# Optimization experiments

Hardware: AMD Instinct MI355X
Metric: run time of the kernel (lower is better)

## Reference

```python
import jax, jax.numpy as jnp
import numpy as np

N = 100000      # nodes
E = 1600000     # edges (avg degree 16)
D_IN, D_H, D_OUT = 128, 128, 64


def setup_inputs() -> dict:
    key = jax.random.key(0)
    k1, k2, k3, k4 = jax.random.split(key, 4)
    x = jax.random.normal(k1, (N, D_IN), dtype=jnp.float32)
    edge_index = jax.random.randint(k2, (2, E), 0, N, dtype=jnp.int32)
    W1 = jax.random.normal(k3, (D_IN, D_H), dtype=jnp.float32) * (1.0 / np.sqrt(D_IN))
    b1 = jnp.zeros((D_H,), dtype=jnp.float32)
    W2 = jax.random.normal(k4, (D_H, D_OUT), dtype=jnp.float32) * (1.0 / np.sqrt(D_H))
    b2 = jnp.zeros((D_OUT,), dtype=jnp.float32)
    return {"x": x, "edge_index": edge_index, "W1": W1, "b1": b1, "W2": W2, "b2": b2}


def _gcn_conv(x, src, dst, W, b):
    """PyG GCNConv: out = D^{-1/2} (A + I) D^{-1/2} (x W) + b."""
    n = x.shape[0]
    h = x @ W  # [N, D_out] — transform first, then aggregate (PyG order)
    loops = jnp.arange(n, dtype=src.dtype)
    src_f = jnp.concatenate([src, loops])
    dst_f = jnp.concatenate([dst, loops])
    deg = jax.ops.segment_sum(jnp.ones_like(dst_f, dtype=h.dtype), dst_f, num_segments=n)
    dinv = jax.lax.rsqrt(deg)  # deg >= 1 due to self-loops
    norm = dinv[src_f] * dinv[dst_f]            # [E+N]
    msg = h[src_f] * norm[:, None]              # [E+N, D_out] gather
    out = jax.ops.segment_sum(msg, dst_f, num_segments=n)  # scatter-add
    return out + b


def reference(x, edge_index, W1, b1, W2, b2):
    src, dst = edge_index[0], edge_index[1]
    h = jax.nn.relu(_gcn_conv(x, src, dst, W1, b1))
    o = _gcn_conv(h, src, dst, W2, b2)
    return jax.nn.log_softmax(o, axis=1)
```

## Files before the change

### kernel.cpp

```cpp
#include <hip/hip_runtime.h>
#include <hip/hip_bf16.h>

typedef __hip_bfloat16 bf16;
typedef short short8 __attribute__((ext_vector_type(8)));
typedef float f32x4 __attribute__((ext_vector_type(4)));

#define NPB 256
#define MAXBUK 1024

__device__ __forceinline__ float bf2f_raw(unsigned short u) {
    unsigned x = ((unsigned)u) << 16; float f; __builtin_memcpy(&f, &x, 4); return f;
}
__device__ __forceinline__ unsigned short f2bf_raw(float f) {
    unsigned u; __builtin_memcpy(&u, &f, 4);
    u += 0x7FFFu + ((u >> 16) & 1u);
    return (unsigned short)(u >> 16);
}
__device__ __forceinline__ float lo_f(unsigned u) {
    unsigned x = u << 16; float f; __builtin_memcpy(&f, &x, 4); return f;
}
__device__ __forceinline__ float hi_f(unsigned u) {
    unsigned x = u & 0xffff0000u; float f; __builtin_memcpy(&f, &x, 4); return f;
}


__global__ __launch_bounds__(1024) void sniff_kernel(const unsigned short* __restrict__ w,
                                                     int nshorts, int* __restrict__ flag) {
    __shared__ int red[1024];
    const int t = threadIdx.x;
    int c = 0;
    for (int i = t; i < nshorts; i += 1024) {
        unsigned e = (w[i] >> 7) & 0xFFu;
        if (e >= 140u || (e >= 1u && e <= 40u)) c++;
    }
    red[t] = c;
    __syncthreads();
    for (int o = 512; o > 0; o >>= 1) {
        if (t < o) red[t] += red[t + o];
        __syncthreads();
    }
    if (t == 0) *flag = (red[0] > nshorts / 8) ? 1 : 0;
}


__global__ __launch_bounds__(256) void prep_kernel(const void* __restrict__ W1p,
                                                   const void* __restrict__ W2p,
                                                   const void* __restrict__ b1p,
                                                   const void* __restrict__ b2p,
                                                   unsigned short* __restrict__ WB1,
                                                   unsigned short* __restrict__ WB2,
                                                   float* __restrict__ b1f,
                                                   float* __restrict__ b2f,
                                                   const int* __restrict__ flag) {
    const int isf32 = *flag;
    const int t = blockIdx.x * 256 + threadIdx.x;
    const int T1 = 16384, T2 = 8192;
    if (t < T1) {
        int j = t & 7, l = (t >> 3) & 63, f = t >> 9;
        int n = f >> 2, kk = f & 3;
        int k = kk * 32 + (l >> 4) * 8 + j;
        int col = n * 16 + (l & 15);
        WB1[t] = isf32 ? f2bf_raw(((const float*)W1p)[k * 128 + col])
                       : ((const unsigned short*)W1p)[k * 128 + col];
    } else if (t < T1 + T2) {
        int o = t - T1;
        int j = o & 7, l = (o >> 3) & 63, f = o >> 9;
        int n = f >> 2, kk = f & 3;
        int k = kk * 32 + (l >> 4) * 8 + j;
        int col = n * 16 + (l & 15);
        WB2[o] = isf32 ? f2bf_raw(((const float*)W2p)[k * 64 + col])
                       : ((const unsigned short*)W2p)[k * 64 + col];
    } else if (t < T1 + T2 + 128) {
        int o = t - T1 - T2;
        b1f[o] = isf32 ? ((const float*)b1p)[o] : bf2f_raw(((const unsigned short*)b1p)[o]);
    } else if (t < T1 + T2 + 192) {
        int o = t - T1 - T2 - 128;
        b2f[o] = isf32 ? ((const float*)b2p)[o] : bf2f_raw(((const unsigned short*)b2p)[o]);
    }
}


__global__ __launch_bounds__(256) void ms_count_kernel(const int* __restrict__ dst,
                                                       int* __restrict__ bktcnt,
                                                       int E, int nbuk) {
    __shared__ int cnt[MAXBUK];
    const int t = threadIdx.x;
    const int e0 = blockIdx.x * 4096;
    const int e1 = min(E, e0 + 4096);
    for (int b = t; b < nbuk; b += 256) cnt[b] = 0;
    __syncthreads();
    for (int e = e0 + t; e < e1; e += 256) atomicAdd(&cnt[dst[e] >> 8], 1);
    __syncthreads();
    for (int b = t; b < nbuk; b += 256) {
        int c = cnt[b];
        if (c) atomicAdd(&bktcnt[b], c);
    }
}

__global__ __launch_bounds__(1024) void bscan_kernel(const int* __restrict__ bktcnt,
                                                     int* __restrict__ bofs,
                                                     int* __restrict__ bcur,
                                                     int* __restrict__ rofs,
                                                     int nbuk, int n, int total) {
    __shared__ int ps[1024];
    const int t = threadIdx.x;
    int v = (t < nbuk) ? bktcnt[t] : 0;
    ps[t] = v;
    __syncthreads();
    for (int o = 1; o < 1024; o <<= 1) {
        int u = (t >= o) ? ps[t - o] : 0;
        __syncthreads();
        ps[t] += u;
        __syncthreads();
    }
    if (t < nbuk) {
        int ex = ps[t] - v;
        bofs[t] = ex;
        bcur[t] = ex;
    }
    if (t == 0) {
        bofs[nbuk] = total;
        rofs[n] = total;
    }
}

__global__ __launch_bounds__(256) void ms_scatter_kernel(const int* __restrict__ src,
                                                         const int* __restrict__ dst,
                                                         int* __restrict__ bcur,
                                                         unsigned* __restrict__ packed,
                                                         int E, int nbuk) {
    __shared__ int cnt[MAXBUK];
    __shared__ int gbase[MAXBUK];
    const int t = threadIdx.x;
    const int e0 = blockIdx.x * 4096;
    const int e1 = min(E, e0 + 4096);
    for (int b = t; b < nbuk; b += 256) cnt[b] = 0;
    __syncthreads();
    for (int e = e0 + t; e < e1; e += 256) atomicAdd(&cnt[dst[e] >> 8], 1);
    __syncthreads();
    for (int b = t; b < nbuk; b += 256) {
        int c = cnt[b];
        gbase[b] = c ? atomicAdd(&bcur[b], c) : 0;
        cnt[b] = 0;
    }
    __syncthreads();
    for (int e = e0 + t; e < e1; e += 256) {
        int d = dst[e];
        int b = d >> 8;
        int r = atomicAdd(&cnt[b], 1);
        packed[gbase[b] + r] = ((unsigned)(d & 255) << 24) | (unsigned)src[e];
    }
}

__global__ __launch_bounds__(256) void csr_fine2_kernel(const unsigned* __restrict__ packed,
                                                        const int* __restrict__ bofs,
                                                        int* __restrict__ rofs,
                                                        float* __restrict__ dinv,
                                                        int* __restrict__ csrc, int n) {
    __shared__ int cnt2[NPB];
    __shared__ int cur[NPB];
    const int t = threadIdx.x;
    const int b = blockIdx.x;
    const int node0 = b << 8;
    const int nn = min(NPB, n - node0);
    cnt2[t] = 0;
    __syncthreads();
    const int beg = bofs[b], end = bofs[b + 1];
    for (int i = beg + t; i < end; i += 256) atomicAdd(&cnt2[packed[i] >> 24], 1);
    __syncthreads();
    int c = cnt2[t];
    cur[t] = c;
    __syncthreads();
    for (int o = 1; o < 256; o <<= 1) {
        int u = (t >= o) ? cur[t - o] : 0;
        __syncthreads();
        cur[t] += u;
        __syncthreads();
    }
    const int base = beg + cur[t] - c;
    if (t < nn) {
        rofs[node0 + t] = base;
        dinv[node0 + t] = rsqrtf((float)(c + 1));
    }
    __syncthreads();
    cur[t] = base;
    __syncthreads();
    for (int i = beg + t; i < end; i += 256) {
        unsigned u = packed[i];
        int pos = atomicAdd(&cur[u >> 24], 1);
        csrc[pos] = (int)(u & 0xFFFFFFu);
    }
}


__global__ __launch_bounds__(256) void gemm1_mfma(const void* __restrict__ Xp,
                                                  const unsigned short* __restrict__ WB1,
                                                  unsigned short* __restrict__ H, int nrows,
                                                  const int* __restrict__ flag) {
    __shared__ __align__(16) unsigned short Xs[128 * 136];
    __shared__ __align__(16) unsigned short Cs[128 * 68];
    const int t = threadIdx.x;
    const int r0 = blockIdx.x * 128;
    const int isf32 = *flag;

    if (isf32) {
        const float4* Xg = (const float4*)Xp;
        #pragma unroll
        for (int i = 0; i < 16; ++i) {
            int idx = t + 256 * i;
            int row = idx >> 5, c4 = idx & 31;
            float4 v = {0.f, 0.f, 0.f, 0.f};
            if (r0 + row < nrows) v = Xg[(size_t)(r0 + row) * 32 + c4];
            unsigned lo = (unsigned)f2bf_raw(v.x) | ((unsigned)f2bf_raw(v.y) << 16);
            unsigned hi = (unsigned)f2bf_raw(v.z) | ((unsigned)f2bf_raw(v.w) << 16);
            *reinterpret_cast<uint2*>(&Xs[row * 136 + c4 * 4]) = make_uint2(lo, hi);
        }
    } else {
        const uint4* Xg = (const uint4*)Xp;
        #pragma unroll
        for (int i = 0; i < 8; ++i) {
            int idx = t + 256 * i;
            int row = idx >> 4, c8 = idx & 15;
            uint4 v = {0u, 0u, 0u, 0u};
            if (r0 + row < nrows) v = Xg[(size_t)(r0 + row) * 16 + c8];
            *reinterpret_cast<uint4*>(&Xs[row * 136 + c8 * 8]) = v;
        }
    }
    __syncthreads();

    const int lane = t & 63, w = t >> 6;
    const int m0 = w * 32;
    short8 a[2][4];
    #pragma unroll
    for (int rt = 0; rt < 2; ++rt)
        #pragma unroll
        for (int kk = 0; kk < 4; ++kk)
            a[rt][kk] = *reinterpret_cast<const short8*>(
                &Xs[(m0 + rt * 16 + (lane & 15)) * 136 + kk * 32 + (lane >> 4) * 8]);

    for (int p = 0; p < 2; ++p) {
        short8 b[4][4];
        #pragma unroll
        for (int n = 0; n < 4; ++n)
            #pragma unroll
            for (int kk = 0; kk < 4; ++kk)
                b[n][kk] = *reinterpret_cast<const short8*>(
                    WB1 + (size_t)(((p * 4 + n) * 4 + kk) * 64 + lane) * 8);
        f32x4 acc[2][4];
        #pragma unroll
        for (int rt = 0; rt < 2; ++rt)
            #pragma unroll
            for (int n = 0; n < 4; ++n) {
                acc[rt][n] = (f32x4){0.f, 0.f, 0.f, 0.f};
                #pragma unroll
                for (int kk = 0; kk < 4; ++kk)
                    acc[rt][n] = __builtin_amdgcn_mfma_f32_16x16x32_bf16(
                        a[rt][kk], b[n][kk], acc[rt][n], 0, 0, 0);
            }
        if (p) __syncthreads();
        #pragma unroll
        for (int rt = 0; rt < 2; ++rt)
            #pragma unroll
            for (int n = 0; n < 4; ++n)
                #pragma unroll
                for (int r = 0; r < 4; ++r) {
                    int row = m0 + rt * 16 + (lane >> 4) * 4 + r;
                    Cs[row * 68 + n * 16 + (lane & 15)] = f2bf_raw(acc[rt][n][r]);
                }
        __syncthreads();
        #pragma unroll
        for (int i = 0; i < 8; ++i) {
            int idx = t + 256 * i;
            int row = idx >> 4, c4 = idx & 15;
            if (r0 + row < nrows) {
                uint2 v = *reinterpret_cast<const uint2*>(&Cs[row * 68 + c4 * 4]);
                *reinterpret_cast<uint2*>(H + (size_t)(r0 + row) * 128 + p * 64 + c4 * 4) = v;
            }
        }
        if (!p) __syncthreads();
    }
}


template <bool RELU_BIAS>
__global__ __launch_bounds__(256) void agg128_v2(const unsigned* __restrict__ H32,
                                                 const int* __restrict__ rofs,
                                                 const int* __restrict__ csrc,
                                                 const float* __restrict__ dinv,
                                                 const float* __restrict__ biasf,
                                                 unsigned* __restrict__ G32, int n) {
    const int lane = threadIdx.x & 63;
    const int node = blockIdx.x * 4 + (threadIdx.x >> 6);
    if (node >= n) return;
    const float di = dinv[node];
    unsigned u = H32[(size_t)node * 64 + lane];
    const float dii = di * di;
    float a0 = dii * lo_f(u), a1 = dii * hi_f(u);
    int j = rofs[node];
    const int end = rofs[node + 1];
    for (; j + 3 < end; j += 4) {
        int s0 = csrc[j], s1 = csrc[j + 1], s2 = csrc[j + 2], s3 = csrc[j + 3];
        float w0 = di * dinv[s0], w1 = di * dinv[s1];
        float w2 = di * dinv[s2], w3 = di * dinv[s3];
        unsigned v0 = H32[(size_t)s0 * 64 + lane];
        unsigned v1 = H32[(size_t)s1 * 64 + lane];
        unsigned v2 = H32[(size_t)s2 * 64 + lane];
        unsigned v3 = H32[(size_t)s3 * 64 + lane];
        a0 = fmaf(w0, lo_f(v0), a0); a1 = fmaf(w0, hi_f(v0), a1);
        a0 = fmaf(w1, lo_f(v1), a0); a1 = fmaf(w1, hi_f(v1), a1);
        a0 = fmaf(w2, lo_f(v2), a0); a1 = fmaf(w2, hi_f(v2), a1);
        a0 = fmaf(w3, lo_f(v3), a0); a1 = fmaf(w3, hi_f(v3), a1);
    }
    for (; j < end; ++j) {
        int s = csrc[j];
        float w = di * dinv[s];
        unsigned v = H32[(size_t)s * 64 + lane];
        a0 = fmaf(w, lo_f(v), a0);
        a1 = fmaf(w, hi_f(v), a1);
    }
    if (RELU_BIAS) {
        a0 = fmaxf(a0 + biasf[2 * lane], 0.f);
        a1 = fmaxf(a1 + biasf[2 * lane + 1], 0.f);
    }
    G32[(size_t)node * 64 + lane] = (unsigned)f2bf_raw(a0) | ((unsigned)f2bf_raw(a1) << 16);
}


__global__ __launch_bounds__(256) void gemm2_mfma(const unsigned short* __restrict__ X,
                                                  const unsigned short* __restrict__ WB2,
                                                  const float* __restrict__ b2f,
                                                  void* __restrict__ OUTv, int nrows,
                                                  const int* __restrict__ flag) {
    __shared__ __align__(16) unsigned short Xs[128 * 136];
    const int t = threadIdx.x;
    const int r0 = blockIdx.x * 128;
    const int outf32 = *flag;

    const uint4* Xg = (const uint4*)X;
    #pragma unroll
    for (int i = 0; i < 8; ++i) {
        int idx = t + 256 * i;
        int row = idx >> 4, c8 = idx & 15;
        uint4 v = {0u, 0u, 0u, 0u};
        if (r0 + row < nrows) v = Xg[(size_t)(r0 + row) * 16 + c8];
        *reinterpret_cast<uint4*>(&Xs[row * 136 + c8 * 8]) = v;
    }
    __syncthreads();

    const int lane = t & 63, w = t >> 6;
    const int m0 = w * 32;
    short8 a[2][4];
    #pragma unroll
    for (int rt = 0; rt < 2; ++rt)
        #pragma unroll
        for (int kk = 0; kk < 4; ++kk)
            a[rt][kk] = *reinterpret_cast<const short8*>(
                &Xs[(m0 + rt * 16 + (lane & 15)) * 136 + kk * 32 + (lane >> 4) * 8]);

    short8 b[4][4];
    #pragma unroll
    for (int n = 0; n < 4; ++n)
        #pragma unroll
        for (int kk = 0; kk < 4; ++kk)
            b[n][kk] = *reinterpret_cast<const short8*>(
                WB2 + (size_t)((n * 4 + kk) * 64 + lane) * 8);

    f32x4 acc[2][4];
    #pragma unroll
    for (int rt = 0; rt < 2; ++rt)
        #pragma unroll
        for (int n = 0; n < 4; ++n) {
            acc[rt][n] = (f32x4){0.f, 0.f, 0.f, 0.f};
            #pragma unroll
            for (int kk = 0; kk < 4; ++kk)
                acc[rt][n] = __builtin_amdgcn_mfma_f32_16x16x32_bf16(
                    a[rt][kk], b[n][kk], acc[rt][n], 0, 0, 0);
        }

    float bc[4];
    #pragma unroll
    for (int n = 0; n < 4; ++n) bc[n] = b2f[n * 16 + (lane & 15)];
    #pragma unroll
    for (int rt = 0; rt < 2; ++rt)
        #pragma unroll
        for (int n = 0; n < 4; ++n)
            #pragma unroll
            for (int r = 0; r < 4; ++r) acc[rt][n][r] += bc[n];

    float lse[2][4];
    #pragma unroll
    for (int rt = 0; rt < 2; ++rt)
        #pragma unroll
        for (int r = 0; r < 4; ++r) {
            float m = fmaxf(fmaxf(acc[rt][0][r], acc[rt][1][r]),
                            fmaxf(acc[rt][2][r], acc[rt][3][r]));
            #pragma unroll
            for (int o = 1; o < 16; o <<= 1) m = fmaxf(m, __shfl_xor(m, o, 64));
            float s = __expf(acc[rt][0][r] - m) + __expf(acc[rt][1][r] - m) +
                      __expf(acc[rt][2][r] - m) + __expf(acc[rt][3][r] - m);
            #pragma unroll
            for (int o = 1; o < 16; o <<= 1) s += __shfl_xor(s, o, 64);
            lse[rt][r] = m + __logf(s);
        }

    const int colb = lane & 15, q = lane >> 4;
    #pragma unroll
    for (int rt = 0; rt < 2; ++rt)
        #pragma unroll
        for (int r = 0; r < 4; ++r) {
            int grow = r0 + m0 + rt * 16 + q * 4 + r;
            if (grow < nrows) {
                if (outf32) {
                    float* Of = (float*)OUTv;
                    #pragma unroll
                    for (int n = 0; n < 4; ++n)
                        Of[(size_t)grow * 64 + n * 16 + colb] = acc[rt][n][r] - lse[rt][r];
                } else {
                    unsigned short* Ob = (unsigned short*)OUTv;
                    #pragma unroll
                    for (int n = 0; n < 4; ++n)
                        Ob[(size_t)grow * 64 + n * 16 + colb] = f2bf_raw(acc[rt][n][r] - lse[rt][r]);
                }
            }
        }
}


extern "C" void kernel_launch(void* const* d_in, const int* in_sizes, int n_in,
                              void* d_out, int out_size, void* d_ws, size_t ws_size,
                              hipStream_t stream) {
    const void* x  = d_in[0];
    const int*  ei = (const int*)d_in[1];
    const void* W1 = d_in[2];
    const void* b1 = d_in[3];
    const void* W2 = d_in[4];
    const void* b2 = d_in[5];

    const int N = in_sizes[0] / 128;
    const int E = in_sizes[1] / 2;
    const int* src = ei;
    const int* dst = ei + E;
    const int NBUK = (N + NPB - 1) / NPB;

    char* p = (char*)d_ws;
    auto alloc = [&](size_t bytes) { char* q = p; p += (bytes + 255) & ~255ull; return q; };
    int*   flag   = (int*)  alloc(4);
    int*   rofs   = (int*)  alloc((size_t)(N + 1) * 4);
    float* dinv   = (float*)alloc((size_t)N * 4);
    int*   bktcnt = (int*)  alloc((size_t)NBUK * 4);
    int*   bofs   = (int*)  alloc((size_t)(NBUK + 1) * 4);
    int*   bcur   = (int*)  alloc((size_t)NBUK * 4);
    float* b1f    = (float*)alloc(128 * 4);
    float* b2f    = (float*)alloc(64 * 4);
    unsigned short* WB1 = (unsigned short*)alloc(16384 * 2);
    unsigned short* WB2 = (unsigned short*)alloc(8192 * 2);
    unsigned* big = (unsigned*)alloc((size_t)N * 128 * 2);
    unsigned* packed = (unsigned*)d_out;
    int*      csrc   = (int*)d_out + E;
    unsigned* g1 = (unsigned*)d_in[0];
    (void)ws_size; (void)n_in; (void)out_size;

    hipMemsetAsync(bktcnt, 0, (size_t)NBUK * 4, stream);
    sniff_kernel<<<1, 1024, 0, stream>>>((const unsigned short*)W1, in_sizes[2], flag);
    prep_kernel<<<97, 256, 0, stream>>>(W1, W2, b1, b2, WB1, WB2, b1f, b2f, flag);
    const int MSB = (E + 4095) / 4096;
    ms_count_kernel<<<MSB, 256, 0, stream>>>(dst, bktcnt, E, NBUK);
    bscan_kernel<<<1, 1024, 0, stream>>>(bktcnt, bofs, bcur, rofs, NBUK, N, E);
    ms_scatter_kernel<<<MSB, 256, 0, stream>>>(src, dst, bcur, packed, E, NBUK);
    csr_fine2_kernel<<<NBUK, 256, 0, stream>>>(packed, bofs, rofs, dinv, csrc, N);

    const int GB = (N + 127) / 128;
    gemm1_mfma<<<GB, 256, 0, stream>>>(x, WB1, (unsigned short*)big, N, flag);
    agg128_v2<true><<<(N + 3) / 4, 256, 0, stream>>>(big, rofs, csrc, dinv, b1f, g1, N);
    agg128_v2<false><<<(N + 3) / 4, 256, 0, stream>>>(g1, rofs, csrc, dinv, nullptr, big, N);
    gemm2_mfma<<<GB, 256, 0, stream>>>((const unsigned short*)big, WB2, b2f, d_out, N, flag);
}
```

Before: 345.1 us.

## Aggregate four edges per wave with 16-byte loads and precomputed source weights

The aggregation kernels now split each 64-lane wave into four 16-lane groups. Each group gathers a different neighbor row with uint4 loads, and the partial sums are combined with cross-lane shuffles. A new pass writes dinv[csrc] per edge into the free region of the output buffer, which removes the dependent dinv gather from the inner loop. The aim is more memory-level parallelism and wider loads in the gather-heavy SpMM. The cost is an extra kernel, shuffle reductions, and only a quarter of lanes doing the store.

```diff
diff --git a/kernel.cpp b/kernel.cpp
--- a/kernel.cpp
+++ b/kernel.cpp
@@ -192,6 +192,13 @@
     }
 }
 
+__global__ __launch_bounds__(256) void wsrc_kernel(const int* __restrict__ csrc,
+                                                   const float* __restrict__ dinv,
+                                                   float* __restrict__ wsrc, int E) {
+    int i = blockIdx.x * 256 + threadIdx.x;
+    if (i < E) wsrc[i] = dinv[csrc[i]];
+}
+
 
 __global__ __launch_bounds__(256) void gemm1_mfma(const void* __restrict__ Xp,
                                                   const unsigned short* __restrict__ WB1,
@@ -282,47 +289,90 @@
 }
 
 
+__device__ __forceinline__ void acc8(float* acc, uint4 v, float w) {
+    acc[0] = fmaf(w, lo_f(v.x), acc[0]); acc[1] = fmaf(w, hi_f(v.x), acc[1]);
+    acc[2] = fmaf(w, lo_f(v.y), acc[2]); acc[3] = fmaf(w, hi_f(v.y), acc[3]);
+    acc[4] = fmaf(w, lo_f(v.z), acc[4]); acc[5] = fmaf(w, hi_f(v.z), acc[5]);
+    acc[6] = fmaf(w, lo_f(v.w), acc[6]); acc[7] = fmaf(w, hi_f(v.w), acc[7]);
+}
+
 template <bool RELU_BIAS>
-__global__ __launch_bounds__(256) void agg128_v2(const unsigned* __restrict__ H32,
+__global__ __launch_bounds__(256) void agg128_v3(const uint4* __restrict__ H4,
                                                  const int* __restrict__ rofs,
                                                  const int* __restrict__ csrc,
+                                                 const float* __restrict__ wsrc,
                                                  const float* __restrict__ dinv,
                                                  const float* __restrict__ biasf,
-                                                 unsigned* __restrict__ G32, int n) {
+                                                 uint4* __restrict__ G4, int n) {
     const int lane = threadIdx.x & 63;
+    const int g = lane >> 4;
+    const int sub = lane & 15;
     const int node = blockIdx.x * 4 + (threadIdx.x >> 6);
     if (node >= n) return;
     const float di = dinv[node];
-    unsigned u = H32[(size_t)node * 64 + lane];
-    const float dii = di * di;
-    float a0 = dii * lo_f(u), a1 = dii * hi_f(u);
+
+    float acc[8];
+    {
+        const float ws = (g == 0) ? di * di : 0.f;
+        uint4 v = H4[(size_t)node * 16 + sub];
+        acc[0] = ws * lo_f(v.x); acc[1] = ws * hi_f(v.x);
+        acc[2] = ws * lo_f(v.y); acc[3] = ws * hi_f(v.y);
+        acc[4] = ws * lo_f(v.z); acc[5] = ws * hi_f(v.z);
+        acc[6] = ws * lo_f(v.w); acc[7] = ws * hi_f(v.w);
+    }
+
     int j = rofs[node];
     const int end = rofs[node + 1];
+
+    for (; j + 7 < end; j += 8) {
+        int s0 = csrc[j + g];
+        int s1 = csrc[j + 4 + g];
+        float w0 = di * wsrc[j + g];
+        float w1 = di * wsrc[j + 4 + g];
+        uint4 v0 = H4[(size_t)s0 * 16 + sub];
+        uint4 v1 = H4[(size_t)s1 * 16 + sub];
+        acc8(acc, v0, w0);
+        acc8(acc, v1, w1);
+    }
     for (; j + 3 < end; j += 4) {
-        int s0 = csrc[j], s1 = csrc[j + 1], s2 = csrc[j + 2], s3 = csrc[j + 3];
-        float w0 = di * dinv[s0], w1 = di * dinv[s1];
-        float w2 = di * dinv[s2], w3 = di * dinv[s3];
-        unsigned v0 = H32[(size_t)s0 * 64 + lane];
-        unsigned v1 = H32[(size_t)s1 * 64 + lane];
-        unsigned v2 = H32[(size_t)s2 * 64 + lane];
-        unsigned v3 = H32[(size_t)s3 * 64 + lane];
-        a0 = fmaf(w0, lo_f(v0), a0); a1 = fmaf(w0, hi_f(v0), a1);
-        a0 = fmaf(w1, lo_f(v1), a0); a1 = fmaf(w1, hi_f(v1), a1);
-        a0 = fmaf(w2, lo_f(v2), a0); a1 = fmaf(w2, hi_f(v2), a1);
-        a0 = fmaf(w3, lo_f(v3), a0); a1 = fmaf(w3, hi_f(v3), a1);
-    }
-    for (; j < end; ++j) {
-        int s = csrc[j];
-        float w = di * dinv[s];
-        unsigned v = H32[(size_t)s * 64 + lane];
-        a0 = fmaf(w, lo_f(v), a0);
-        a1 = fmaf(w, hi_f(v), a1);
-    }
-    if (RELU_BIAS) {
-        a0 = fmaxf(a0 + biasf[2 * lane], 0.f);
-        a1 = fmaxf(a1 + biasf[2 * lane + 1], 0.f);
-    }
-    G32[(size_t)node * 64 + lane] = (unsigned)f2bf_raw(a0) | ((unsigned)f2bf_raw(a1) << 16);
+        int s0 = csrc[j + g];
+        float w0 = di * wsrc[j + g];
+        uint4 v0 = H4[(size_t)s0 * 16 + sub];
+        acc8(acc, v0, w0);
+    }
+    if (j + g < end) {
+        int s0 = csrc[j + g];
+        float w0 = di * wsrc[j + g];
+        uint4 v0 = H4[(size_t)s0 * 16 + sub];
+        acc8(acc, v0, w0);
+    }
+
+    #pragma unroll
+    for (int i = 0; i < 8; ++i) {
+        acc[i] += __shfl_xor(acc[i], 16, 64);
+        acc[i] += __shfl_xor(acc[i], 32, 64);
+    }
+
+    if (g == 0) {
+        if (RELU_BIAS) {
+            const float4* b4 = (const float4*)biasf;
+            float4 blo = b4[sub * 2], bhi = b4[sub * 2 + 1];
+            acc[0] = fmaxf(acc[0] + blo.x, 0.f);
+            acc[1] = fmaxf(acc[1] + blo.y, 0.f);
+            acc[2] = fmaxf(acc[2] + blo.z, 0.f);
+            acc[3] = fmaxf(acc[3] + blo.w, 0.f);
+            acc[4] = fmaxf(acc[4] + bhi.x, 0.f);
+            acc[5] = fmaxf(acc[5] + bhi.y, 0.f);
+            acc[6] = fmaxf(acc[6] + bhi.z, 0.f);
+            acc[7] = fmaxf(acc[7] + bhi.w, 0.f);
+        }
+        uint4 o;
+        o.x = (unsigned)f2bf_raw(acc[0]) | ((unsigned)f2bf_raw(acc[1]) << 16);
+        o.y = (unsigned)f2bf_raw(acc[2]) | ((unsigned)f2bf_raw(acc[3]) << 16);
+        o.z = (unsigned)f2bf_raw(acc[4]) | ((unsigned)f2bf_raw(acc[5]) << 16);
+        o.w = (unsigned)f2bf_raw(acc[6]) | ((unsigned)f2bf_raw(acc[7]) << 16);
+        G4[(size_t)node * 16 + sub] = o;
+    }
 }
 
 
@@ -456,6 +506,7 @@
     unsigned short* WB2 = (unsigned short*)alloc(8192 * 2);
     unsigned* big = (unsigned*)alloc((size_t)N * 128 * 2);
     unsigned* packed = (unsigned*)d_out;
+    float*    wsrc   = (float*)d_out;
     int*      csrc   = (int*)d_out + E;
     unsigned* g1 = (unsigned*)d_in[0];
     (void)ws_size; (void)n_in; (void)out_size;
@@ -468,10 +519,11 @@
     bscan_kernel<<<1, 1024, 0, stream>>>(bktcnt, bofs, bcur, rofs, NBUK, N, E);
     ms_scatter_kernel<<<MSB, 256, 0, stream>>>(src, dst, bcur, packed, E, NBUK);
     csr_fine2_kernel<<<NBUK, 256, 0, stream>>>(packed, bofs, rofs, dinv, csrc, N);
+    wsrc_kernel<<<(E + 255) / 256, 256, 0, stream>>>(csrc, dinv, wsrc, E);
 
     const int GB = (N + 127) / 128;
     gemm1_mfma<<<GB, 256, 0, stream>>>(x, WB1, (unsigned short*)big, N, flag);
-    agg128_v2<true><<<(N + 3) / 4, 256, 0, stream>>>(big, rofs, csrc, dinv, b1f, g1, N);
-    agg128_v2<false><<<(N + 3) / 4, 256, 0, stream>>>(g1, rofs, csrc, dinv, nullptr, big, N);
+    agg128_v3<true><<<(N + 3) / 4, 256, 0, stream>>>((const uint4*)big, rofs, csrc, wsrc, dinv, b1f, (uint4*)g1, N);
+    agg128_v3<false><<<(N + 3) / 4, 256, 0, stream>>>((const uint4*)g1, rofs, csrc, wsrc, dinv, nullptr, (uint4*)big, N);
     gemm2_mfma<<<GB, 256, 0, stream>>>((const unsigned short*)big, WB2, b2f, d_out, N, flag);
 }
```

New measurement: 326.6 us. 1.06x faster.
